# Optimization experiments

Measured on AMD Instinct MI355X. Metric: run time of the kernel, lower is better.

## Reference

```python
import jax, jax.numpy as jnp
import numpy as np

SIDE = 32
N_NODES = SIDE * SIDE          # n_nodes = 1024
WIDTH = 128
IN_DIM = 128
T_DIM = 2
U_DIM = 1
BATCH = 8
MSG_STEPS = int(np.sqrt(N_NODES))  # 32
LN_EPS = 1e-5


def _create_grid():
    # matches GEN.create_grid for t_dim == 2
    pos = np.array([[i / (SIDE - 1), j / (SIDE - 1)]
                    for i in range(SIDE) for j in range(SIDE)], dtype=np.float32)
    edges = []
    for i in range(1, SIDE):
        for j in range(1, SIDE):
            a = SIDE * i + j
            b = SIDE * (i - 1) + j
            c = SIDE * i + (j - 1)
            edges += [[a, b], [b, a], [c, a], [a, c]]
    edge_index = np.array(edges, dtype=np.int64).T  # [2, E]
    return pos, edge_index


def setup_inputs() -> dict:
    key = jax.random.key(0)
    ks = jax.random.split(key, 16)
    node_pos_np, edge_index_np = _create_grid()

    def lin(k, fan_in, fan_out):
        kw, kb = jax.random.split(k)
        bound = 1.0 / np.sqrt(fan_in)
        W = jax.random.uniform(kw, (fan_in, fan_out), jnp.float32, -bound, bound)
        b = jax.random.uniform(kb, (fan_out,), jnp.float32, -bound, bound)
        return W, b

    We1, be1 = lin(ks[0], IN_DIM, WIDTH)
    We2, be2 = lin(ks[1], WIDTH, WIDTH)
    We3, be3 = lin(ks[2], WIDTH, WIDTH)
    Wg, bg = lin(ks[3], WIDTH + T_DIM, WIDTH)
    Wd1, bd1 = lin(ks[4], WIDTH + T_DIM, WIDTH)
    Wd2, bd2 = lin(ks[5], WIDTH, WIDTH)
    Wd3, bd3 = lin(ks[6], WIDTH, U_DIM)

    return {
        'X1': jax.random.uniform(ks[7], (BATCH, IN_DIM + T_DIM), jnp.float32),
        'node_pos': jnp.asarray(node_pos_np),
        'edge_index': jnp.asarray(edge_index_np),
        'We1': We1, 'be1': be1, 'We2': We2, 'be2': be2, 'We3': We3, 'be3': be3,
        'Wg': Wg, 'bg': bg,
        'gamma': jnp.ones((WIDTH,), jnp.float32),
        'beta': jnp.zeros((WIDTH,), jnp.float32),
        'Wd1': Wd1, 'bd1': bd1, 'Wd2': Wd2, 'bd2': bd2, 'Wd3': Wd3, 'bd3': bd3,
    }


def _gen_forward(X1, node_pos, edge_index, We1, be1, We2, be2, We3, be3,
                 Wg, bg, gamma, beta, Wd1, bd1, Wd2, bd2, Wd3, bd3):
    s, t = X1[:, :-T_DIM], X1[:, -T_DIM:]

    # encoder MLP: Linear-ReLU-Linear-ReLU-Linear
    h = jax.nn.relu(s @ We1 + be1)
    h = jax.nn.relu(h @ We2 + be2)
    enc = h @ We3 + be3                                   # [B, W]

    # per-sample graph construction: softmax over node distance to origin
    # (identical for every sample), node_features = weight @ enc[i][None,:]
    d0 = jnp.sqrt(jnp.sum(node_pos ** 2, axis=1, keepdims=True))  # [N,1]
    w0 = jax.nn.softmax(-d0, axis=0)                              # [N,1]
    x = w0[None, :, :] * enc[:, None, :]                          # [B,N,W]

    # GCNConv normalization with added self-loops (symmetric norm)
    row, col = edge_index[0], edge_index[1]
    deg = jnp.ones((N_NODES,), x.dtype).at[col].add(1.0)
    dinv = deg ** -0.5
    enorm = dinv[row] * dinv[col]   # edge norm
    snorm = dinv * dinv             # self-loop norm
    posb = jnp.broadcast_to(node_pos[None], (x.shape[0], N_NODES, T_DIM))

    def step(xc, _):
        xin = jnp.concatenate([posb, xc], axis=-1)        # [B,N,W+2]
        xw = xin @ Wg                                     # [B,N,W]
        msgs = enorm[None, :, None] * xw[:, row, :]       # [B,E,W]
        agg = (snorm[None, :, None] * xw).at[:, col, :].add(msgs) + bg
        xn = xc + agg
        mu = jnp.mean(xn, axis=-1, keepdims=True)
        var = jnp.var(xn, axis=-1, keepdims=True)
        xn = (xn - mu) * jax.lax.rsqrt(var + LN_EPS) * gamma + beta
        return xn, None

    x, _ = jax.lax.scan(step, x, None, length=MSG_STEPS)  # [B,N,W]

    # readout: softmax over node distance to query point t
    dist = jnp.sqrt(jnp.sum((node_pos[None] - t[:, None, :]) ** 2,
                            axis=2, keepdims=True))       # [B,N,1]
    wt = jax.nn.softmax(-dist, axis=1)                    # [B,N,1]
    hidden = jnp.einsum('bnk,bnw->bw', wt, x)             # [B,W]
    hidden = jnp.concatenate([hidden, t], axis=1)

    h = jax.nn.relu(hidden @ Wd1 + bd1)
    h = jax.nn.relu(h @ Wd2 + bd2)
    y = (h @ Wd3 + bd3).squeeze()                         # [B] (u_dim == 1)
    return y


def reference(X1, node_pos, edge_index, We1, be1, We2, be2, We3, be3,
              Wg, bg, gamma, beta, Wd1, bd1, Wd2, bd2, Wd3, bd3):
    return _gen_forward(X1, node_pos, edge_index, We1, be1, We2, be2, We3, be3,
                        Wg, bg, gamma, beta, Wd1, bd1, Wd2, bd2, Wd3, bd3)
```

## Files before the change

### kernel.cpp

```cpp
#include <hip/hip_runtime.h>

#define NODES 1024
#define WD    128
#define NSTEPS 32
#define LNEPS 1e-5f

typedef __bf16 bf16x8 __attribute__((ext_vector_type(8)));
typedef float  f32x4  __attribute__((ext_vector_type(4)));
typedef int    i32x4  __attribute__((ext_vector_type(4)));

__device__ __forceinline__ f32x4 mfma16(i32x4 a, i32x4 b, f32x4 c) {
  return __builtin_amdgcn_mfma_f32_16x16x32_bf16(
      __builtin_bit_cast(bf16x8, a), __builtin_bit_cast(bf16x8, b), c, 0, 0, 0);
}

__device__ __forceinline__ unsigned short f2bf(float f) {
  union { float f; unsigned u; } v; v.f = f;
  unsigned r = v.u + 0x7FFF + ((v.u >> 16) & 1);
  return (unsigned short)(r >> 16);
}
__device__ __forceinline__ float bf2f(unsigned short h) {
  union { unsigned u; float f; } v; v.u = ((unsigned)h) << 16;
  return v.f;
}

__device__ __forceinline__ float dinv_of(int n) {
  const int i = n >> 5, j = n & 31;
  int cnt = 1;
  cnt += (i >= 1 && j >= 1) ? 1 : 0;
  cnt += (i <= 30 && j >= 1) ? 1 : 0;
  cnt += (i >= 1 && j >= 1) ? 1 : 0;
  cnt += (i >= 1 && j <= 30) ? 1 : 0;
  return 1.f / sqrtf((float)cnt);
}

__device__ __forceinline__ int halo_node(int h, int v0) {
  const int i0 = v0 >> 5, j0 = v0 & 31;
  int u;
  bool valid;
  if (h < 4)       { u = v0 + h;             valid = true; }
  else if (h == 4) { u = v0 - 1;             valid = (j0 >= 1); }
  else if (h == 5) { u = v0 + 4;             valid = (j0 + 4 <= 31); }
  else if (h < 10) { u = v0 - 32 + (h - 6);  valid = (i0 >= 1); }
  else             { u = v0 + 32 + (h - 10); valid = (i0 <= 30); }
  return valid ? u : v0;
}

__device__ __forceinline__ void agg_row(const float* __restrict__ Xin, int u,
                                        int j, int c0, float* __restrict__ z) {
  const float dv = dinv_of(u);
  const float dvv = dv * dv;
  const int iu = u >> 5, ju = u & 31;
  const bool exu[4] = {iu >= 1 && ju >= 1, iu <= 30 && ju >= 1,
                       iu >= 1 && ju >= 1, iu >= 1 && ju <= 30};
  const int dd[4] = {-32, 32, -1, 1};
  {
    const float* xs = Xin + (size_t)((j << 10) + u) * WD + c0;
    const float4 a0 = *(const float4*)(xs);
    const float4 a1 = *(const float4*)(xs + 4);
    z[0] = dvv * a0.x; z[1] = dvv * a0.y; z[2] = dvv * a0.z; z[3] = dvv * a0.w;
    z[4] = dvv * a1.x; z[5] = dvv * a1.y; z[6] = dvv * a1.z; z[7] = dvv * a1.w;
  }
#pragma unroll
  for (int e = 0; e < 4; e++) {
    const int u2 = exu[e] ? u + dd[e] : u;
    const float w = exu[e] ? dinv_of(u2) * dv : 0.f;
    const float* nr = Xin + (size_t)((j << 10) + u2) * WD + c0;
    const float4 t0 = *(const float4*)(nr);
    const float4 t1 = *(const float4*)(nr + 4);
    z[0] += w * t0.x; z[1] += w * t0.y; z[2] += w * t0.z; z[3] += w * t0.w;
    z[4] += w * t1.x; z[5] += w * t1.y; z[6] += w * t1.z; z[7] += w * t1.w;
  }
}

__device__ __forceinline__ void cvt8(const float* __restrict__ xn, i32x4& hi,
                                     i32x4& lo) {
  int hw[4], lw[4];
#pragma unroll
  for (int d = 0; d < 4; d++) {
    const unsigned short ha = f2bf(xn[2 * d]);
    const unsigned short hb = f2bf(xn[2 * d + 1]);
    hw[d] = (int)ha | ((int)hb << 16);
    lw[d] = (int)f2bf(xn[2 * d] - bf2f(ha)) |
            ((int)f2bf(xn[2 * d + 1] - bf2f(hb)) << 16);
  }
  hi = i32x4{hw[0], hw[1], hw[2], hw[3]};
  lo = i32x4{lw[0], lw[1], lw[2], lw[3]};
}

__device__ __forceinline__ void lay512(const float* __restrict__ W,
                                       const float* __restrict__ bias,
                                       const float* __restrict__ src,
                                       float* __restrict__ dst, int tid,
                                       bool relu_) {
  const int c = tid & 127;
  const int b0 = tid >> 7;
  float a0 = bias ? bias[c] : 0.f;
  float a1 = a0;
#pragma unroll 8
  for (int k = 0; k < WD; k++) {
    const float wv = W[k * WD + c];
    a0 += src[b0 * WD + k] * wv;
    a1 += src[(b0 + 4) * WD + k] * wv;
  }
  dst[b0 * WD + c] = relu_ ? fmaxf(a0, 0.f) : a0;
  dst[(b0 + 4) * WD + c] = relu_ ? fmaxf(a1, 0.f) : a1;
  __syncthreads();
}

__global__ __launch_bounds__(512) void init_kernel(
    const float* __restrict__ X1, const float* __restrict__ pos,
    const float* __restrict__ We1, const float* __restrict__ be1,
    const float* __restrict__ We2, const float* __restrict__ be2,
    const float* __restrict__ We3, const float* __restrict__ be3,
    const float* __restrict__ Wg, const float* __restrict__ bg,
    float* __restrict__ X, float* __restrict__ Q, int* __restrict__ Bpk) {
  __shared__ float ioA[1024];
  __shared__ float ioB[1024];
  __shared__ float red[512];
  const int tid = threadIdx.x;
  const int v0 = blockIdx.x * 4;
  const float* W2 = Wg + 2 * WD;

  for (int i = tid; i < 1024; i += 512) ioA[i] = X1[(i >> 7) * 130 + (i & 127)];
  __syncthreads();
  lay512(We1, be1, ioA, ioB, tid, true);
  lay512(We2, be2, ioB, ioA, tid, true);
  lay512(We3, be3, ioA, ioB, tid, false);

  {
    float es = 0.f;
#pragma unroll
    for (int r = 0; r < 2; r++) {
      const int n = tid + 512 * r;
      const float px = pos[2 * n], py = pos[2 * n + 1];
      es += expf(-sqrtf(px * px + py * py));
    }
    red[tid] = es;
  }
  __syncthreads();
  for (int s = 256; s > 0; s >>= 1) {
    if (tid < s) red[tid] += red[tid + s];
    __syncthreads();
  }
  const float w0sum = red[0];

  {
    const int lr = tid >> 4, cq = tid & 15, c0 = cq * 8;
    const int b = lr >> 2, nl = lr & 3, v = v0 + nl;
    const int grow = (b << 10) + v;
    const float pxv = pos[2 * v], pyv = pos[2 * v + 1];
    const float w0v = expf(-sqrtf(pxv * pxv + pyv * pyv)) / w0sum;
#pragma unroll
    for (int q4 = 0; q4 < 2; q4++) {
      const float4 e = *(const float4*)(ioB + b * WD + c0 + 4 * q4);
      *(float4*)(X + (size_t)grow * WD + c0 + 4 * q4) =
          make_float4(w0v * e.x, w0v * e.y, w0v * e.z, w0v * e.w);
    }
  }
  {
    const int vq = v0 + (tid >> 7);
    const int cc = tid & 127;
    const float dv = dinv_of(vq);
    const float dvv = dv * dv;
    const int iv = vq >> 5, jv = vq & 31;
    float cx = dvv * pos[2 * vq], cy = dvv * pos[2 * vq + 1];
    const bool ex[4] = {(iv >= 1) && (jv >= 1), (iv <= 30) && (jv >= 1),
                        (iv >= 1) && (jv >= 1), (iv >= 1) && (jv <= 30)};
    const int du[4] = {-32, 32, -1, 1};
#pragma unroll
    for (int e = 0; e < 4; e++) {
      if (ex[e]) {
        const int u = vq + du[e];
        const float w = dinv_of(u) * dv;
        cx += w * pos[2 * u];
        cy += w * pos[2 * u + 1];
      }
    }
    Q[vq * WD + cc] = bg[cc] + cx * Wg[cc] + cy * Wg[WD + cc];
  }
  if (tid < 64) {
    const int e = blockIdx.x * 64 + tid;
    const int nt = e >> 11, l = (e >> 5) & 63, half = (e >> 4) & 1;
    const int kt = (e >> 2) & 3, d = e & 3;
    const int k0 = 32 * kt + ((l >> 4) << 3) + 2 * d;
    const int n = 16 * nt + (l & 15);
    const float w0_ = W2[k0 * WD + n];
    const float w1_ = W2[(k0 + 1) * WD + n];
    const unsigned short h0 = f2bf(w0_), h1 = f2bf(w1_);
    int val;
    if (half == 0) {
      val = (int)h0 | ((int)h1 << 16);
    } else {
      val = (int)f2bf(w0_ - bf2f(h0)) | ((int)f2bf(w1_ - bf2f(h1)) << 16);
    }
    Bpk[e] = val;
  }
}

__global__ __launch_bounds__(512) void pair_kernel(
    const float* __restrict__ Xin, float* __restrict__ Xout,
    const int* __restrict__ Bpk, const float* __restrict__ Q,
    const float* __restrict__ gamma, const float* __restrict__ beta) {
  __shared__ int BIG[15232];
  __shared__ int R3[4352];
  const int tid = threadIdx.x;
  const int v0 = blockIdx.x * 4;
  const int wv = tid >> 6, l = tid & 63;

  i32x4 bh[4], bl[4];
  {
    const int lb0 = (wv * 64 + l) * 32;
#pragma unroll
    for (int kt = 0; kt < 4; kt++) {
      bh[kt] = *(const i32x4*)(Bpk + lb0 + kt * 4);
      bl[kt] = *(const i32x4*)(Bpk + lb0 + 16 + kt * 4);
    }
  }
  const int cq = tid & 15, c0 = cq * 8;
  float gmm[8], btt[8];
#pragma unroll
  for (int q = 0; q < 8; q++) {
    gmm[q] = gamma[c0 + q];
    btt[q] = beta[c0 + q];
  }

#pragma unroll 1
  for (int it = 0; it < 4; it++) {
    const int idx = tid + it * 512;
    if (idx < 1792) {
      const int row = idx >> 4;
      const int h = row >> 3, j = row & 7;
      const int u = halo_node(h, v0);
      float z[8];
      agg_row(Xin, u, j, c0, z);
      i32x4 hi, lo;
      cvt8(z, hi, lo);
      const int ab = row * 68 + cq * 4;
      *(i32x4*)(BIG + ab) = hi;
      *(i32x4*)(BIG + 7616 + ab) = lo;
    }
  }
  __syncthreads();

  f32x4 acc1[7] = {};
  {
    const int g4 = (l >> 4) << 2;
    const int mr = l & 15;
#pragma unroll
    for (int kt = 0; kt < 4; kt++) {
      const int off = 16 * kt + g4;
#pragma unroll
      for (int mt = 0; mt < 7; mt++) {
        const int rb = (mt * 16 + mr) * 68 + off;
        const i32x4 ah = *(const i32x4*)(BIG + rb);
        const i32x4 al = *(const i32x4*)(BIG + 7616 + rb);
        acc1[mt] = mfma16(ah, bh[kt], acc1[mt]);
        acc1[mt] = mfma16(ah, bl[kt], acc1[mt]);
        acc1[mt] = mfma16(al, bh[kt], acc1[mt]);
      }
    }
  }
  __syncthreads();
  {
    float* ZW = (float*)BIG;
    const int colb = 16 * wv + (l & 15);
    const int rbase = (l >> 4) << 2;
#pragma unroll
    for (int mt = 0; mt < 7; mt++)
#pragma unroll
      for (int r = 0; r < 4; r++)
        ZW[(mt * 16 + rbase + r) * 132 + colb] = acc1[mt][r];
  }
  __syncthreads();

#pragma unroll 1
  for (int it = 0; it < 4; it++) {
    const int idx = tid + it * 512;
    if (idx < 1792) {
      const int row = idx >> 4;
      const int h = row >> 3, j = row & 7;
      const int u = halo_node(h, v0);
      float* ZW = (float*)BIG;
      float* zs = ZW + row * 132 + c0;
      const float* xs = Xin + (size_t)((j << 10) + u) * WD + c0;
      const float* qs = Q + u * WD + c0;
      float y[8];
      {
        const float4 z0 = *(const float4*)(zs);
        const float4 z1 = *(const float4*)(zs + 4);
        const float4 a0 = *(const float4*)(xs);
        const float4 a1 = *(const float4*)(xs + 4);
        const float4 q0 = *(const float4*)(qs);
        const float4 q1 = *(const float4*)(qs + 4);
        y[0] = a0.x + q0.x + z0.x; y[1] = a0.y + q0.y + z0.y;
        y[2] = a0.z + q0.z + z0.z; y[3] = a0.w + q0.w + z0.w;
        y[4] = a1.x + q1.x + z1.x; y[5] = a1.y + q1.y + z1.y;
        y[6] = a1.z + q1.z + z1.z; y[7] = a1.w + q1.w + z1.w;
      }
      float s1 = 0.f, s2 = 0.f;
#pragma unroll
      for (int q = 0; q < 8; q++) { s1 += y[q]; s2 += y[q] * y[q]; }
#pragma unroll
      for (int m = 1; m < 16; m <<= 1) {
        s1 += __shfl_xor(s1, m);
        s2 += __shfl_xor(s2, m);
      }
      const float mu = s1 * (1.f / 128.f);
      const float var = s2 * (1.f / 128.f) - mu * mu;
      const float rs = 1.f / sqrtf(var + LNEPS);
#pragma unroll
      for (int q = 0; q < 8; q++)
        zs[q] = (y[q] - mu) * rs * gmm[q] + btt[q];
    }
  }
  __syncthreads();

  const int lr = tid >> 4;
  const int bb = lr >> 2, nl = lr & 3, v = v0 + nl;
  float xown[8], qown[8];
  {
    const float* X1f = (const float*)BIG;
    const float dv = dinv_of(v);
    const float dvv = dv * dv;
    const int iv = v >> 5, jv = v & 31;
    const bool exv[4] = {iv >= 1 && jv >= 1, iv <= 30 && jv >= 1,
                         iv >= 1 && jv >= 1, iv >= 1 && jv <= 30};
    const int du[4] = {-32, 32, -1, 1};
    const int hn[4] = {6 + nl, 10 + nl, (nl == 0) ? 4 : nl - 1,
                       (nl == 3) ? 5 : nl + 1};
    const float* os = X1f + (nl * 8 + bb) * 132 + c0;
    float z2[8];
#pragma unroll
    for (int q = 0; q < 8; q++) {
      xown[q] = os[q];
      z2[q] = dvv * xown[q];
    }
#pragma unroll
    for (int e = 0; e < 4; e++) {
      const float w = exv[e] ? dinv_of(v + du[e]) * dv : 0.f;
      const float* nr = X1f + (hn[e] * 8 + bb) * 132 + c0;
#pragma unroll
      for (int q = 0; q < 8; q++) z2[q] += w * nr[q];
    }
    {
      const float* qs = Q + v * WD + c0;
#pragma unroll
      for (int q = 0; q < 8; q++) qown[q] = qs[q];
    }
    i32x4 hi, lo;
    cvt8(z2, hi, lo);
    const int ab = lr * 68 + cq * 4;
    *(i32x4*)(R3 + ab) = hi;
    *(i32x4*)(R3 + 2176 + ab) = lo;
  }
  __syncthreads();

  f32x4 acc2[2] = {};
  {
    const int g4 = (l >> 4) << 2;
    const int mr0 = (l & 15) * 68;
    const int mr1 = mr0 + 16 * 68;
#pragma unroll
    for (int kt = 0; kt < 4; kt++) {
      const int off = 16 * kt + g4;
      const i32x4 ah0 = *(const i32x4*)(R3 + mr0 + off);
      const i32x4 ah1 = *(const i32x4*)(R3 + mr1 + off);
      const i32x4 al0 = *(const i32x4*)(R3 + 2176 + mr0 + off);
      const i32x4 al1 = *(const i32x4*)(R3 + 2176 + mr1 + off);
      acc2[0] = mfma16(ah0, bh[kt], acc2[0]);
      acc2[1] = mfma16(ah1, bh[kt], acc2[1]);
      acc2[0] = mfma16(ah0, bl[kt], acc2[0]);
      acc2[1] = mfma16(ah1, bl[kt], acc2[1]);
      acc2[0] = mfma16(al0, bh[kt], acc2[0]);
      acc2[1] = mfma16(al1, bh[kt], acc2[1]);
    }
  }
  __syncthreads();
  {
    float* ZW2 = (float*)R3;
    const int colb = 16 * wv + (l & 15);
    const int rbase = (l >> 4) << 2;
#pragma unroll
    for (int mt = 0; mt < 2; mt++)
#pragma unroll
      for (int r = 0; r < 4; r++)
        ZW2[(16 * mt + rbase + r) * 132 + colb] = acc2[mt][r];
  }
  __syncthreads();

  {
    const float* ZW2 = (const float*)R3;
    const float* zs = ZW2 + lr * 132 + c0;
    float y[8];
#pragma unroll
    for (int q = 0; q < 8; q++) y[q] = xown[q] + qown[q] + zs[q];
    float s1 = 0.f, s2 = 0.f;
#pragma unroll
    for (int q = 0; q < 8; q++) { s1 += y[q]; s2 += y[q] * y[q]; }
#pragma unroll
    for (int m = 1; m < 16; m <<= 1) {
      s1 += __shfl_xor(s1, m);
      s2 += __shfl_xor(s2, m);
    }
    const float mu = s1 * (1.f / 128.f);
    const float var = s2 * (1.f / 128.f) - mu * mu;
    const float rs = 1.f / sqrtf(var + LNEPS);
    float xn[8];
#pragma unroll
    for (int q = 0; q < 8; q++) xn[q] = (y[q] - mu) * rs * gmm[q] + btt[q];
    float* xo = Xout + (size_t)((bb << 10) + v) * WD + c0;
    *(float4*)(xo) = make_float4(xn[0], xn[1], xn[2], xn[3]);
    *(float4*)(xo + 4) = make_float4(xn[4], xn[5], xn[6], xn[7]);
  }
}

__global__ __launch_bounds__(1024) void hiddec_kernel(
    const float* __restrict__ pos, const float* __restrict__ X1,
    const float* __restrict__ Xf, const float* __restrict__ Wd1,
    const float* __restrict__ bd1, const float* __restrict__ Wd2,
    const float* __restrict__ bd2, const float* __restrict__ Wd3,
    const float* __restrict__ bd3, float* __restrict__ out) {
  __shared__ float wsh[NODES];
  __shared__ float red[16];
  __shared__ float asum[8][WD];
  __shared__ float hid[132];
  __shared__ float hh[WD];
  const int b = blockIdx.x;
  const int n = threadIdx.x;
  const float tx = X1[b * 130 + 128], ty = X1[b * 130 + 129];
  const float px = pos[2 * n] - tx, py = pos[2 * n + 1] - ty;
  const float e = expf(-sqrtf(px * px + py * py));
  float s = e;
#pragma unroll
  for (int m = 32; m >= 1; m >>= 1) s += __shfl_xor(s, m);
  if ((n & 63) == 0) red[n >> 6] = s;
  __syncthreads();
  float tot = 0.f;
#pragma unroll
  for (int w = 0; w < 16; w++) tot += red[w];
  wsh[n] = e / tot;
  __syncthreads();
  const int c = n & 127, g = n >> 7;
  {
    const float* xp = Xf + ((size_t)b * NODES + g * 128) * WD + c;
    const float* wp = wsh + g * 128;
    float a = 0.f;
#pragma unroll 4
    for (int it = 0; it < 128; it++) a += wp[it] * xp[it * WD];
    asum[g][c] = a;
  }
  __syncthreads();
  if (g == 0) {
    float t2 = asum[0][c];
#pragma unroll
    for (int gg = 1; gg < 8; gg++) t2 += asum[gg][c];
    hid[c] = t2;
  }
  if (n == 0) { hid[128] = tx; hid[129] = ty; }
  __syncthreads();
  float a1v = 0.f;
  if (n < 128) {
    a1v = bd1[n];
    for (int k = 0; k < 130; k++) a1v += hid[k] * Wd1[k * WD + n];
  }
  __syncthreads();
  if (n < 128) hh[n] = fmaxf(a1v, 0.f);
  __syncthreads();
  float p = 0.f;
  if (n < 128) {
    float a2 = bd2[n];
#pragma unroll 8
    for (int k = 0; k < WD; k++) a2 += hh[k] * Wd2[k * WD + n];
    p = fmaxf(a2, 0.f) * Wd3[n];
  }
#pragma unroll
  for (int m = 32; m >= 1; m >>= 1) p += __shfl_xor(p, m);
  if ((n & 63) == 0) red[n >> 6] = p;
  __syncthreads();
  if (n == 0) out[b] = red[0] + red[1] + bd3[0];
}

extern "C" void kernel_launch(void* const* d_in, const int* in_sizes, int n_in,
                              void* d_out, int out_size, void* d_ws,
                              size_t ws_size, hipStream_t stream) {
  const float* X1 = (const float*)d_in[0];
  const float* pos = (const float*)d_in[1];
  const float* We1 = (const float*)d_in[3];
  const float* be1 = (const float*)d_in[4];
  const float* We2 = (const float*)d_in[5];
  const float* be2 = (const float*)d_in[6];
  const float* We3 = (const float*)d_in[7];
  const float* be3 = (const float*)d_in[8];
  const float* Wg = (const float*)d_in[9];
  const float* bg = (const float*)d_in[10];
  const float* gamma = (const float*)d_in[11];
  const float* beta = (const float*)d_in[12];
  const float* Wd1 = (const float*)d_in[13];
  const float* bd1 = (const float*)d_in[14];
  const float* Wd2 = (const float*)d_in[15];
  const float* bd2 = (const float*)d_in[16];
  const float* Wd3 = (const float*)d_in[17];
  const float* bd3 = (const float*)d_in[18];
  float* out = (float*)d_out;
  float* f = (float*)d_ws;

  float* Q = f;
  int* Bpk = (int*)(f + 131072);
  float* Xa = f + 147456;
  float* Xb = f + 1196032;

  init_kernel<<<256, 512, 0, stream>>>(X1, pos, We1, be1, We2, be2, We3, be3,
                                       Wg, bg, Xa, Q, Bpk);
  for (int p = 0; p < NSTEPS / 2; p++) {
    const float* xin = (p & 1) ? Xb : Xa;
    float* xout = (p & 1) ? Xa : Xb;
    pair_kernel<<<256, 512, 0, stream>>>(xin, xout, Bpk, Q, gamma, beta);
  }
  hiddec_kernel<<<8, 1024, 0, stream>>>(pos, X1, Xa, Wd1, bd1, Wd2, bd2, Wd3,
                                        bd3, out);
  (void)in_sizes;
  (void)n_in;
  (void)out_size;
  (void)ws_size;
}
```

Baseline: 293.3 us.

## Keep halo rows in registers across aggregation and LayerNorm in pair_kernel

Each thread now owns up to two full halo rows of 16 channels (8 threads per row) instead of looping over 8-channel slices. It loads the self, Q and four neighbour rows once into registers and reuses the self and Q values in the first LayerNorm, so the second global read of Xin and Q is gone. The second stage reuses Q0 and reads X1 from shared memory, and launch bounds are set to one block per SM to allow more registers. The cost is much higher register pressure and only 256 threads active in the final stages, and it relies on row0 for tid<256 lining up with the own node for Q reuse.

```diff
diff --git a/kernel.cpp b/kernel.cpp
--- a/kernel.cpp
+++ b/kernel.cpp
@@ -44,33 +44,6 @@
   else if (h < 10) { u = v0 - 32 + (h - 6);  valid = (i0 >= 1); }
   else             { u = v0 + 32 + (h - 10); valid = (i0 <= 30); }
   return valid ? u : v0;
-}
-
-__device__ __forceinline__ void agg_row(const float* __restrict__ Xin, int u,
-                                        int j, int c0, float* __restrict__ z) {
-  const float dv = dinv_of(u);
-  const float dvv = dv * dv;
-  const int iu = u >> 5, ju = u & 31;
-  const bool exu[4] = {iu >= 1 && ju >= 1, iu <= 30 && ju >= 1,
-                       iu >= 1 && ju >= 1, iu >= 1 && ju <= 30};
-  const int dd[4] = {-32, 32, -1, 1};
-  {
-    const float* xs = Xin + (size_t)((j << 10) + u) * WD + c0;
-    const float4 a0 = *(const float4*)(xs);
-    const float4 a1 = *(const float4*)(xs + 4);
-    z[0] = dvv * a0.x; z[1] = dvv * a0.y; z[2] = dvv * a0.z; z[3] = dvv * a0.w;
-    z[4] = dvv * a1.x; z[5] = dvv * a1.y; z[6] = dvv * a1.z; z[7] = dvv * a1.w;
-  }
-#pragma unroll
-  for (int e = 0; e < 4; e++) {
-    const int u2 = exu[e] ? u + dd[e] : u;
-    const float w = exu[e] ? dinv_of(u2) * dv : 0.f;
-    const float* nr = Xin + (size_t)((j << 10) + u2) * WD + c0;
-    const float4 t0 = *(const float4*)(nr);
-    const float4 t1 = *(const float4*)(nr + 4);
-    z[0] += w * t0.x; z[1] += w * t0.y; z[2] += w * t0.z; z[3] += w * t0.w;
-    z[4] += w * t1.x; z[5] += w * t1.y; z[6] += w * t1.z; z[7] += w * t1.w;
-  }
 }
 
 __device__ __forceinline__ void cvt8(const float* __restrict__ xn, i32x4& hi,
@@ -198,7 +171,7 @@
   }
 }
 
-__global__ __launch_bounds__(512) void pair_kernel(
+__global__ __launch_bounds__(512, 1) void pair_kernel(
     const float* __restrict__ Xin, float* __restrict__ Xout,
     const int* __restrict__ Bpk, const float* __restrict__ Q,
     const float* __restrict__ gamma, const float* __restrict__ beta) {
@@ -217,29 +190,142 @@
       bl[kt] = *(const i32x4*)(Bpk + lb0 + 16 + kt * 4);
     }
   }
-  const int cq = tid & 15, c0 = cq * 8;
-  float gmm[8], btt[8];
-#pragma unroll
-  for (int q = 0; q < 8; q++) {
-    gmm[q] = gamma[c0 + q];
-    btt[q] = beta[c0 + q];
-  }
-
-#pragma unroll 1
-  for (int it = 0; it < 4; it++) {
-    const int idx = tid + it * 512;
-    if (idx < 1792) {
-      const int row = idx >> 4;
-      const int h = row >> 3, j = row & 7;
-      const int u = halo_node(h, v0);
-      float z[8];
-      agg_row(Xin, u, j, c0, z);
-      i32x4 hi, lo;
-      cvt8(z, hi, lo);
-      const int ab = row * 68 + cq * 4;
-      *(i32x4*)(BIG + ab) = hi;
-      *(i32x4*)(BIG + 7616 + ab) = lo;
-    }
+  const int cq = tid & 7, c0 = cq * 16;
+  float gmm[16], btt[16];
+#pragma unroll
+  for (int q4 = 0; q4 < 4; q4++) {
+    const float4 gg = *(const float4*)(gamma + c0 + 4 * q4);
+    const float4 bb = *(const float4*)(beta + c0 + 4 * q4);
+    gmm[4 * q4] = gg.x; gmm[4 * q4 + 1] = gg.y;
+    gmm[4 * q4 + 2] = gg.z; gmm[4 * q4 + 3] = gg.w;
+    btt[4 * q4] = bb.x; btt[4 * q4 + 1] = bb.y;
+    btt[4 * q4 + 2] = bb.z; btt[4 * q4 + 3] = bb.w;
+  }
+
+  const int row0 = tid >> 3;
+  const int row1 = row0 + 64;
+  const bool has1 = (tid < 384);
+
+  const int h0 = row0 >> 3, jb0 = row0 & 7;
+  const int u0 = halo_node(h0, v0);
+  const float dv0 = dinv_of(u0);
+  const float ws0 = dv0 * dv0;
+  float wn0[4];
+  int un0[4];
+  {
+    const int iu = u0 >> 5, ju = u0 & 31;
+    const bool ex[4] = {iu >= 1 && ju >= 1, iu <= 30 && ju >= 1,
+                        iu >= 1 && ju >= 1, iu >= 1 && ju <= 30};
+    const int dd[4] = {-32, 32, -1, 1};
+#pragma unroll
+    for (int e = 0; e < 4; e++) {
+      un0[e] = ex[e] ? u0 + dd[e] : u0;
+      wn0[e] = ex[e] ? dinv_of(un0[e]) * dv0 : 0.f;
+    }
+  }
+  float4 S0[4], Q0[4], N0a[4], N0b[4], N0c[4], N0d[4];
+  {
+    const float* xs = Xin + (size_t)((jb0 << 10) + u0) * WD + c0;
+    const float* qs = Q + u0 * WD + c0;
+    const float* na = Xin + (size_t)((jb0 << 10) + un0[0]) * WD + c0;
+    const float* nb = Xin + (size_t)((jb0 << 10) + un0[1]) * WD + c0;
+    const float* nc = Xin + (size_t)((jb0 << 10) + un0[2]) * WD + c0;
+    const float* nd = Xin + (size_t)((jb0 << 10) + un0[3]) * WD + c0;
+#pragma unroll
+    for (int q4 = 0; q4 < 4; q4++) {
+      S0[q4] = *(const float4*)(xs + 4 * q4);
+      Q0[q4] = *(const float4*)(qs + 4 * q4);
+      N0a[q4] = *(const float4*)(na + 4 * q4);
+      N0b[q4] = *(const float4*)(nb + 4 * q4);
+      N0c[q4] = *(const float4*)(nc + 4 * q4);
+      N0d[q4] = *(const float4*)(nd + 4 * q4);
+    }
+  }
+  float ws1 = 0.f, wn1[4] = {0.f, 0.f, 0.f, 0.f};
+  float4 S1[4], Q1[4], N1a[4], N1b[4], N1c[4], N1d[4];
+  if (has1) {
+    const int h1 = row1 >> 3, jb1 = row1 & 7;
+    const int u1 = halo_node(h1, v0);
+    const float dv1 = dinv_of(u1);
+    ws1 = dv1 * dv1;
+    int un1[4];
+    const int iu = u1 >> 5, ju = u1 & 31;
+    const bool ex[4] = {iu >= 1 && ju >= 1, iu <= 30 && ju >= 1,
+                        iu >= 1 && ju >= 1, iu >= 1 && ju <= 30};
+    const int dd[4] = {-32, 32, -1, 1};
+#pragma unroll
+    for (int e = 0; e < 4; e++) {
+      un1[e] = ex[e] ? u1 + dd[e] : u1;
+      wn1[e] = ex[e] ? dinv_of(un1[e]) * dv1 : 0.f;
+    }
+    const float* xs = Xin + (size_t)((jb1 << 10) + u1) * WD + c0;
+    const float* qs = Q + u1 * WD + c0;
+    const float* na = Xin + (size_t)((jb1 << 10) + un1[0]) * WD + c0;
+    const float* nb = Xin + (size_t)((jb1 << 10) + un1[1]) * WD + c0;
+    const float* nc = Xin + (size_t)((jb1 << 10) + un1[2]) * WD + c0;
+    const float* nd = Xin + (size_t)((jb1 << 10) + un1[3]) * WD + c0;
+#pragma unroll
+    for (int q4 = 0; q4 < 4; q4++) {
+      S1[q4] = *(const float4*)(xs + 4 * q4);
+      Q1[q4] = *(const float4*)(qs + 4 * q4);
+      N1a[q4] = *(const float4*)(na + 4 * q4);
+      N1b[q4] = *(const float4*)(nb + 4 * q4);
+      N1c[q4] = *(const float4*)(nc + 4 * q4);
+      N1d[q4] = *(const float4*)(nd + 4 * q4);
+    }
+  }
+
+  {
+    float z[16];
+#pragma unroll
+    for (int q4 = 0; q4 < 4; q4++) {
+      z[4 * q4 + 0] = ws0 * S0[q4].x + wn0[0] * N0a[q4].x +
+                      wn0[1] * N0b[q4].x + wn0[2] * N0c[q4].x +
+                      wn0[3] * N0d[q4].x;
+      z[4 * q4 + 1] = ws0 * S0[q4].y + wn0[0] * N0a[q4].y +
+                      wn0[1] * N0b[q4].y + wn0[2] * N0c[q4].y +
+                      wn0[3] * N0d[q4].y;
+      z[4 * q4 + 2] = ws0 * S0[q4].z + wn0[0] * N0a[q4].z +
+                      wn0[1] * N0b[q4].z + wn0[2] * N0c[q4].z +
+                      wn0[3] * N0d[q4].z;
+      z[4 * q4 + 3] = ws0 * S0[q4].w + wn0[0] * N0a[q4].w +
+                      wn0[1] * N0b[q4].w + wn0[2] * N0c[q4].w +
+                      wn0[3] * N0d[q4].w;
+    }
+    i32x4 hi0, lo0, hi1, lo1;
+    cvt8(z, hi0, lo0);
+    cvt8(z + 8, hi1, lo1);
+    const int ab = row0 * 68 + cq * 8;
+    *(i32x4*)(BIG + ab) = hi0;
+    *(i32x4*)(BIG + ab + 4) = hi1;
+    *(i32x4*)(BIG + 7616 + ab) = lo0;
+    *(i32x4*)(BIG + 7616 + ab + 4) = lo1;
+  }
+  if (has1) {
+    float z[16];
+#pragma unroll
+    for (int q4 = 0; q4 < 4; q4++) {
+      z[4 * q4 + 0] = ws1 * S1[q4].x + wn1[0] * N1a[q4].x +
+                      wn1[1] * N1b[q4].x + wn1[2] * N1c[q4].x +
+                      wn1[3] * N1d[q4].x;
+      z[4 * q4 + 1] = ws1 * S1[q4].y + wn1[0] * N1a[q4].y +
+                      wn1[1] * N1b[q4].y + wn1[2] * N1c[q4].y +
+                      wn1[3] * N1d[q4].y;
+      z[4 * q4 + 2] = ws1 * S1[q4].z + wn1[0] * N1a[q4].z +
+                      wn1[1] * N1b[q4].z + wn1[2] * N1c[q4].z +
+                      wn1[3] * N1d[q4].z;
+      z[4 * q4 + 3] = ws1 * S1[q4].w + wn1[0] * N1a[q4].w +
+                      wn1[1] * N1b[q4].w + wn1[2] * N1c[q4].w +
+                      wn1[3] * N1d[q4].w;
+    }
+    i32x4 hi0, lo0, hi1, lo1;
+    cvt8(z, hi0, lo0);
+    cvt8(z + 8, hi1, lo1);
+    const int ab = row1 * 68 + cq * 8;
+    *(i32x4*)(BIG + ab) = hi0;
+    *(i32x4*)(BIG + ab + 4) = hi1;
+    *(i32x4*)(BIG + 7616 + ab) = lo0;
+    *(i32x4*)(BIG + 7616 + ab + 4) = lo1;
   }
   __syncthreads();
 
@@ -274,35 +360,24 @@
   }
   __syncthreads();
 
-#pragma unroll 1
-  for (int it = 0; it < 4; it++) {
-    const int idx = tid + it * 512;
-    if (idx < 1792) {
-      const int row = idx >> 4;
-      const int h = row >> 3, j = row & 7;
-      const int u = halo_node(h, v0);
-      float* ZW = (float*)BIG;
-      float* zs = ZW + row * 132 + c0;
-      const float* xs = Xin + (size_t)((j << 10) + u) * WD + c0;
-      const float* qs = Q + u * WD + c0;
-      float y[8];
-      {
-        const float4 z0 = *(const float4*)(zs);
-        const float4 z1 = *(const float4*)(zs + 4);
-        const float4 a0 = *(const float4*)(xs);
-        const float4 a1 = *(const float4*)(xs + 4);
-        const float4 q0 = *(const float4*)(qs);
-        const float4 q1 = *(const float4*)(qs + 4);
-        y[0] = a0.x + q0.x + z0.x; y[1] = a0.y + q0.y + z0.y;
-        y[2] = a0.z + q0.z + z0.z; y[3] = a0.w + q0.w + z0.w;
-        y[4] = a1.x + q1.x + z1.x; y[5] = a1.y + q1.y + z1.y;
-        y[6] = a1.z + q1.z + z1.z; y[7] = a1.w + q1.w + z1.w;
+  {
+    float* ZW = (float*)BIG;
+    {
+      float* zs = ZW + row0 * 132 + c0;
+      float y[16];
+#pragma unroll
+      for (int q4 = 0; q4 < 4; q4++) {
+        const float4 zz = *(const float4*)(zs + 4 * q4);
+        y[4 * q4 + 0] = S0[q4].x + Q0[q4].x + zz.x;
+        y[4 * q4 + 1] = S0[q4].y + Q0[q4].y + zz.y;
+        y[4 * q4 + 2] = S0[q4].z + Q0[q4].z + zz.z;
+        y[4 * q4 + 3] = S0[q4].w + Q0[q4].w + zz.w;
       }
       float s1 = 0.f, s2 = 0.f;
 #pragma unroll
-      for (int q = 0; q < 8; q++) { s1 += y[q]; s2 += y[q] * y[q]; }
-#pragma unroll
-      for (int m = 1; m < 16; m <<= 1) {
+      for (int q = 0; q < 16; q++) { s1 += y[q]; s2 += y[q] * y[q]; }
+#pragma unroll
+      for (int m = 1; m < 8; m <<= 1) {
         s1 += __shfl_xor(s1, m);
         s2 += __shfl_xor(s2, m);
       }
@@ -310,17 +385,43 @@
       const float var = s2 * (1.f / 128.f) - mu * mu;
       const float rs = 1.f / sqrtf(var + LNEPS);
 #pragma unroll
-      for (int q = 0; q < 8; q++)
+      for (int q = 0; q < 16; q++)
         zs[q] = (y[q] - mu) * rs * gmm[q] + btt[q];
     }
-  }
-  __syncthreads();
-
-  const int lr = tid >> 4;
-  const int bb = lr >> 2, nl = lr & 3, v = v0 + nl;
-  float xown[8], qown[8];
-  {
+    if (has1) {
+      float* zs = ZW + row1 * 132 + c0;
+      float y[16];
+#pragma unroll
+      for (int q4 = 0; q4 < 4; q4++) {
+        const float4 zz = *(const float4*)(zs + 4 * q4);
+        y[4 * q4 + 0] = S1[q4].x + Q1[q4].x + zz.x;
+        y[4 * q4 + 1] = S1[q4].y + Q1[q4].y + zz.y;
+        y[4 * q4 + 2] = S1[q4].z + Q1[q4].z + zz.z;
+        y[4 * q4 + 3] = S1[q4].w + Q1[q4].w + zz.w;
+      }
+      float s1 = 0.f, s2 = 0.f;
+#pragma unroll
+      for (int q = 0; q < 16; q++) { s1 += y[q]; s2 += y[q] * y[q]; }
+#pragma unroll
+      for (int m = 1; m < 8; m <<= 1) {
+        s1 += __shfl_xor(s1, m);
+        s2 += __shfl_xor(s2, m);
+      }
+      const float mu = s1 * (1.f / 128.f);
+      const float var = s2 * (1.f / 128.f) - mu * mu;
+      const float rs = 1.f / sqrtf(var + LNEPS);
+#pragma unroll
+      for (int q = 0; q < 16; q++)
+        zs[q] = (y[q] - mu) * rs * gmm[q] + btt[q];
+    }
+  }
+  __syncthreads();
+
+  if (tid < 256) {
     const float* X1f = (const float*)BIG;
+    const int lr = tid >> 3;
+    const int nl = lr >> 3, bbt = lr & 7;
+    const int v = v0 + nl;
     const float dv = dinv_of(v);
     const float dvv = dv * dv;
     const int iv = v >> 5, jv = v & 31;
@@ -329,30 +430,27 @@
     const int du[4] = {-32, 32, -1, 1};
     const int hn[4] = {6 + nl, 10 + nl, (nl == 0) ? 4 : nl - 1,
                        (nl == 3) ? 5 : nl + 1};
-    const float* os = X1f + (nl * 8 + bb) * 132 + c0;
-    float z2[8];
-#pragma unroll
-    for (int q = 0; q < 8; q++) {
-      xown[q] = os[q];
-      z2[q] = dvv * xown[q];
+    float z2[16];
+    {
+      const float* os = X1f + lr * 132 + c0;
+#pragma unroll
+      for (int q = 0; q < 16; q++) z2[q] = dvv * os[q];
     }
 #pragma unroll
     for (int e = 0; e < 4; e++) {
       const float w = exv[e] ? dinv_of(v + du[e]) * dv : 0.f;
-      const float* nr = X1f + (hn[e] * 8 + bb) * 132 + c0;
-#pragma unroll
-      for (int q = 0; q < 8; q++) z2[q] += w * nr[q];
-    }
-    {
-      const float* qs = Q + v * WD + c0;
-#pragma unroll
-      for (int q = 0; q < 8; q++) qown[q] = qs[q];
-    }
-    i32x4 hi, lo;
-    cvt8(z2, hi, lo);
-    const int ab = lr * 68 + cq * 4;
-    *(i32x4*)(R3 + ab) = hi;
-    *(i32x4*)(R3 + 2176 + ab) = lo;
+      const float* nr = X1f + (hn[e] * 8 + bbt) * 132 + c0;
+#pragma unroll
+      for (int q = 0; q < 16; q++) z2[q] += w * nr[q];
+    }
+    i32x4 hi0, lo0, hi1, lo1;
+    cvt8(z2, hi0, lo0);
+    cvt8(z2 + 8, hi1, lo1);
+    const int ab = lr * 68 + cq * 8;
+    *(i32x4*)(R3 + ab) = hi0;
+    *(i32x4*)(R3 + ab + 4) = hi1;
+    *(i32x4*)(R3 + 2176 + ab) = lo0;
+    *(i32x4*)(R3 + 2176 + ab + 4) = lo1;
   }
   __syncthreads();
 
@@ -389,29 +487,41 @@
   }
   __syncthreads();
 
-  {
+  if (tid < 256) {
+    const float* X1f = (const float*)BIG;
     const float* ZW2 = (const float*)R3;
+    const int lr = tid >> 3;
+    const int nl = lr >> 3, bbt = lr & 7;
+    const int v = v0 + nl;
+    const float* x1s = X1f + lr * 132 + c0;
     const float* zs = ZW2 + lr * 132 + c0;
-    float y[8];
-#pragma unroll
-    for (int q = 0; q < 8; q++) y[q] = xown[q] + qown[q] + zs[q];
+    float y[16];
+#pragma unroll
+    for (int q4 = 0; q4 < 4; q4++) {
+      y[4 * q4 + 0] = x1s[4 * q4 + 0] + Q0[q4].x + zs[4 * q4 + 0];
+      y[4 * q4 + 1] = x1s[4 * q4 + 1] + Q0[q4].y + zs[4 * q4 + 1];
+      y[4 * q4 + 2] = x1s[4 * q4 + 2] + Q0[q4].z + zs[4 * q4 + 2];
+      y[4 * q4 + 3] = x1s[4 * q4 + 3] + Q0[q4].w + zs[4 * q4 + 3];
+    }
     float s1 = 0.f, s2 = 0.f;
 #pragma unroll
-    for (int q = 0; q < 8; q++) { s1 += y[q]; s2 += y[q] * y[q]; }
-#pragma unroll
-    for (int m = 1; m < 16; m <<= 1) {
+    for (int q = 0; q < 16; q++) { s1 += y[q]; s2 += y[q] * y[q]; }
+#pragma unroll
+    for (int m = 1; m < 8; m <<= 1) {
       s1 += __shfl_xor(s1, m);
       s2 += __shfl_xor(s2, m);
     }
     const float mu = s1 * (1.f / 128.f);
     const float var = s2 * (1.f / 128.f) - mu * mu;
     const float rs = 1.f / sqrtf(var + LNEPS);
-    float xn[8];
-#pragma unroll
-    for (int q = 0; q < 8; q++) xn[q] = (y[q] - mu) * rs * gmm[q] + btt[q];
-    float* xo = Xout + (size_t)((bb << 10) + v) * WD + c0;
-    *(float4*)(xo) = make_float4(xn[0], xn[1], xn[2], xn[3]);
-    *(float4*)(xo + 4) = make_float4(xn[4], xn[5], xn[6], xn[7]);
+    float xn[16];
+#pragma unroll
+    for (int q = 0; q < 16; q++) xn[q] = (y[q] - mu) * rs * gmm[q] + btt[q];
+    float* xo = Xout + (size_t)((bbt << 10) + v) * WD + c0;
+#pragma unroll
+    for (int q4 = 0; q4 < 4; q4++)
+      *(float4*)(xo + 4 * q4) = make_float4(xn[4 * q4], xn[4 * q4 + 1],
+                                            xn[4 * q4 + 2], xn[4 * q4 + 3]);
   }
 }
 
```

Result: slower. 396.2 us (+35.1%).
